# Performance work log

Measured on AMD Instinct MI355X. Metric: run time of the kernel, lower is better.

The kernel has to match this reference:

```python
import jax, jax.numpy as jnp
import numpy as np
import math

B = 128      # n_atom_basis
F = 32       # n_filters
R = 20       # n_rbf
N = 16384    # atoms
E = 262144   # edges
LOG2 = 0.6931471805599453
IS2 = 1.0 / math.sqrt(2.0)
IS3 = 1.0 / math.sqrt(3.0)
IS6 = 1.0 / math.sqrt(6.0)


def ssp(x):
    # shifted softplus: softplus(x) - log(2)
    return jax.nn.softplus(x) - LOG2


def setup_inputs() -> dict:
    key = jax.random.key(0)
    ks = jax.random.split(key, 14)
    return dict(
        x=jax.random.normal(ks[0], (N, 4 * B), jnp.float32),
        idx_i=jax.random.randint(ks[1], (E,), 0, N),
        idx_j=jax.random.randint(ks[2], (E,), 0, N),
        f_ij=jax.random.normal(ks[3], (E, R), jnp.float32),
        rcut_ij=jax.random.uniform(ks[4], (E,), jnp.float32),
        Yr_ij=jax.random.normal(ks[5], (E, 4), jnp.float32),
        # e3nn-style Linear weights (N(0,1), normalized by 1/sqrt(fan_in) at use)
        w_in2f_s=jax.random.normal(ks[6], (B, F), jnp.float32),
        w_in2f_v=jax.random.normal(ks[7], (B, F), jnp.float32),
        W1=jax.random.normal(ks[8], (R, F), jnp.float32) / math.sqrt(R),
        b1=jnp.zeros((F,), jnp.float32),
        W2=jax.random.normal(ks[9], (F, 6 * F), jnp.float32) / math.sqrt(F),
        b2=jnp.zeros((6 * F,), jnp.float32),
        w_f2o1_s=jax.random.normal(ks[10], (2 * F, B), jnp.float32),
        w_f2o1_v=jax.random.normal(ks[11], (2 * F, B), jnp.float32),
        w_f2o2_s=jax.random.normal(ks[12], (B, B), jnp.float32),
        w_f2o2_v=jax.random.normal(ks[13], (B, B), jnp.float32),
    )


def reference(x, idx_i, idx_j, f_ij, rcut_ij, Yr_ij,
              w_in2f_s, w_in2f_v, W1, b1, W2, b2,
              w_f2o1_s, w_f2o1_v, w_f2o2_s, w_f2o2_v):
    n = x.shape[0]
    # input layout: [B x 0e | B x 1o]
    xs = x[:, :B]                          # [N,B] scalars
    xv = x[:, B:].reshape(n, B, 3)         # [N,B,3] vectors
    # in2f: per-l equivariant linear (fan_in = B)
    hs = (xs @ w_in2f_s) / math.sqrt(B)                            # [N,F]
    hv = jnp.einsum('nbc,bf->nfc', xv, w_in2f_v) / math.sqrt(B)    # [N,F,3]
    # gather neighbors j
    s = hs[idx_j]                          # [E,F]
    v = hv[idx_j]                          # [E,F,3]
    ys = Yr_ij[:, 0]                       # [E]   l=0 part of Y(r)
    yv = Yr_ij[:, 1:4]                     # [E,3] l=1 part of Y(r)
    # FullTensorProduct (0e+1o) x (0e+1o), component normalization
    t_s1 = s * ys[:, None]                                   # 0e (0x0)
    t_s2 = jnp.einsum('efc,ec->ef', v, yv) * IS3             # 0e (1x1->0)
    t_v1 = s[:, :, None] * yv[:, None, :]                    # 1o (0x1)
    t_v2 = v * ys[:, None, None]                             # 1o (1x0)
    t_pv = jnp.cross(v, yv[:, None, :]) * IS2                # 1e (1x1->1)
    ax, ay, az = v[..., 0], v[..., 1], v[..., 2]
    bx, by, bz = yv[:, None, 0:1], yv[:, None, 1:2], yv[:, None, 2:3]
    bx, by, bz = bx[..., 0], by[..., 0], bz[..., 0]
    t_q = jnp.stack([                                        # 2e (1x1->2)
        (ax * by + ay * bx) * IS2,
        (ay * bz + az * by) * IS2,
        (2.0 * az * bz - ax * bx - ay * by) * IS6,
        (ax * bz + az * bx) * IS2,
        (ax * bx - ay * by) * IS2,
    ], axis=-1)                                              # [E,F,5]
    # radial filter network -> one scalar per irrep instance (6 per filter)
    h = ssp(f_ij @ W1 + b1)
    Wij = (h @ W2 + b2) * rcut_ij[:, None]                   # [E,6F]
    Wf = Wij.reshape(-1, F, 6)
    # elementwise tensor product (continuous-filter convolution)
    edge = jnp.concatenate([
        (t_s1 * Wf[..., 0])[..., None],
        (t_s2 * Wf[..., 1])[..., None],
        t_v1 * Wf[..., 2:3],
        t_v2 * Wf[..., 3:4],
        t_pv * Wf[..., 4:5],
        t_q * Wf[..., 5:6],
    ], axis=-1)                                              # [E,F,16]
    # scatter-add over center atoms i
    agg = jax.ops.segment_sum(edge.reshape(edge.shape[0], -1), idx_i,
                              num_segments=n).reshape(n, F, 16)
    # f2out_1: e3nn Linear keeps only matching irreps (0e,1o); 1e,2e dropped
    s_in = jnp.concatenate([agg[..., 0], agg[..., 1]], axis=1)          # [N,2F]
    v_in = jnp.concatenate([agg[..., 2:5], agg[..., 5:8]], axis=1)      # [N,2F,3]
    os1 = (s_in @ w_f2o1_s) / math.sqrt(2 * F)
    ov1 = jnp.einsum('nmc,mb->nbc', v_in, w_f2o1_v) / math.sqrt(2 * F)
    # gated activation: ssp on scalars only
    os1 = ssp(os1)
    # f2out_2
    os2 = (os1 @ w_f2o2_s) / math.sqrt(B)
    ov2 = jnp.einsum('nbc,bd->ndc', ov1, w_f2o2_v) / math.sqrt(B)
    return jnp.concatenate([os2, ov2.reshape(n, -1)], axis=-1)          # [N,4B]
```

## Files before the change

kernel.cpp:

```cpp
#include <hip/hip_runtime.h>
#include <math.h>

#define NN 16384
#define BB 128
#define FF 32
#define RR 20
#define EE 262144

__device__ __forceinline__ float sspf(float x) {
  return fmaxf(x, 0.0f) + log1pf(expf(-fabsf(x))) - 0.69314718055994531f;
}

__device__ __forceinline__ unsigned int pack_bf2(float a, float b) {
  unsigned int ua = __float_as_uint(a);
  ua = (ua + 0x7fffu + ((ua >> 16) & 1u)) >> 16;
  unsigned int ub = __float_as_uint(b);
  ub = (ub + 0x7fffu + ((ub >> 16) & 1u)) & 0xffff0000u;
  return ua | ub;
}

__global__ __launch_bounds__(256) void k_embed(const float* __restrict__ x,
        const float* __restrict__ ws, const float* __restrict__ wv,
        float4* __restrict__ hsv) {
  __shared__ float sx[32 * 516];
  int t = threadIdx.x;
  int b0 = blockIdx.x * 32;
  const float4* xg = (const float4*)(x + (size_t)b0 * 512);
  for (int i = t; i < 4096; i += 256) {
    int row = i >> 7, col = i & 127;
    *(float4*)(sx + row * 516 + col * 4) = xg[i];
  }
  __syncthreads();
  int n = t >> 3, fq = t & 7;
  const float* xr = sx + n * 516;
  float acc[4][4];
#pragma unroll
  for (int k = 0; k < 4; k++)
#pragma unroll
    for (int c = 0; c < 4; c++) acc[k][c] = 0.f;
  for (int bq = 0; bq < 32; bq++) {
    float4 xs4 = *(const float4*)(xr + 4 * bq);
    float4 a0 = *(const float4*)(xr + 128 + 12 * bq);
    float4 a1 = *(const float4*)(xr + 128 + 12 * bq + 4);
    float4 a2 = *(const float4*)(xr + 128 + 12 * bq + 8);
    float xsv[4] = {xs4.x, xs4.y, xs4.z, xs4.w};
    float vv[4][3];
    vv[0][0] = a0.x; vv[0][1] = a0.y; vv[0][2] = a0.z;
    vv[1][0] = a0.w; vv[1][1] = a1.x; vv[1][2] = a1.y;
    vv[2][0] = a1.z; vv[2][1] = a1.w; vv[2][2] = a2.x;
    vv[3][0] = a2.y; vv[3][1] = a2.z; vv[3][2] = a2.w;
#pragma unroll
    for (int bb = 0; bb < 4; bb++) {
      int b = 4 * bq + bb;
      float4 w_s = *(const float4*)(ws + b * 32 + 4 * fq);
      float4 w_v = *(const float4*)(wv + b * 32 + 4 * fq);
      float wsx[4] = {w_s.x, w_s.y, w_s.z, w_s.w};
      float wvx[4] = {w_v.x, w_v.y, w_v.z, w_v.w};
#pragma unroll
      for (int k = 0; k < 4; k++) {
        acc[k][0] += xsv[bb] * wsx[k];
        acc[k][1] += vv[bb][0] * wvx[k];
        acc[k][2] += vv[bb][1] * wvx[k];
        acc[k][3] += vv[bb][2] * wvx[k];
      }
    }
  }
  const float sc = 0.088388347648318447f;
#pragma unroll
  for (int k = 0; k < 4; k++) {
    float4 o;
    o.x = acc[k][0] * sc; o.y = acc[k][1] * sc;
    o.z = acc[k][2] * sc; o.w = acc[k][3] * sc;
    hsv[(size_t)(b0 + n) * 32 + 4 * fq + k] = o;
  }
}

__global__ __launch_bounds__(256) void k_count(const int* __restrict__ idx_i,
        int* __restrict__ cnt, int* __restrict__ pos) {
  int e = blockIdx.x * 256 + threadIdx.x;
  pos[e] = atomicAdd(cnt + idx_i[e], 1);
}

__global__ __launch_bounds__(256) void k_scan(const int* __restrict__ cnt,
        int* __restrict__ offs) {
  __shared__ int part[256];
  int t = threadIdx.x;
  int s = 0;
  for (int i = t * 64; i < t * 64 + 64; ++i) s += cnt[i];
  part[t] = s;
  __syncthreads();
  if (t == 0) {
    int run = 0;
    for (int i = 0; i < 256; i++) { int v = part[i]; part[i] = run; run += v; }
    offs[NN] = run;
  }
  __syncthreads();
  int run = part[t];
  for (int i = t * 64; i < t * 64 + 64; ++i) { offs[i] = run; run += cnt[i]; }
}

__global__ __launch_bounds__(256) void k_fill(const int* __restrict__ idx_i,
        const int* __restrict__ idx_j, const float* __restrict__ Yr,
        const int* __restrict__ pos, const int* __restrict__ offs,
        int* __restrict__ slot_of_e, int* __restrict__ idxj_csr,
        float4* __restrict__ Yr_csr) {
  int e = blockIdx.x * 256 + threadIdx.x;
  int slot = offs[idx_i[e]] + pos[e];
  slot_of_e[e] = slot;
  idxj_csr[slot] = idx_j[e];
  Yr_csr[slot] = *(const float4*)(Yr + (size_t)e * 4);
}

__global__ __launch_bounds__(256) void k_wv(const float* __restrict__ w1v,
        const float* __restrict__ w2v, float* __restrict__ Wv) {
  int o = blockIdx.x * 256 + threadIdx.x;
  int m = o >> 7, d = o & 127;
  float s = 0.f;
  for (int b = 0; b < 128; b++) s += w1v[m * 128 + b] * w2v[b * 128 + d];
  Wv[o] = s * 0.011048543456039804f;
}

__global__ __launch_bounds__(256, 4) void k_wab(
        const float* __restrict__ fij, const float* __restrict__ rcut,
        const int* __restrict__ slot_of_e,
        const float* __restrict__ W1, const float* __restrict__ b1,
        const float* __restrict__ W2, const float* __restrict__ b2,
        unsigned int* __restrict__ Wab) {
  __shared__ float sW1[640];
  __shared__ float sb1[32];
  __shared__ float sW2c[4096];
  __shared__ float sb2c[128];
  __shared__ float sfij[20 * 130];
  __shared__ float sh[128 * 37];
  __shared__ float srct[128];
  __shared__ int sslot[128];
  int t = threadIdx.x;
  size_t e0 = (size_t)blockIdx.x * 128;
  for (int i = t; i < 640; i += 256) sW1[i] = W1[i];
  if (t < 32) sb1[t] = b1[t];
  for (int i = t; i < 4096; i += 256) {
    int p = i >> 7, c = i & 127;
    sW2c[i] = W2[p * 192 + 6 * (c >> 2) + (c & 3)];
  }
  if (t < 128) sb2c[t] = b2[6 * (t >> 2) + (t & 3)];
  for (int i = t; i < 2560; i += 256) {
    int el = i / 20, r = i - el * 20;
    sfij[r * 130 + el] = fij[e0 * 20 + i];
  }
  if (t < 128) {
    srct[t] = rcut[e0 + t];
    sslot[t] = slot_of_e[e0 + t];
  }
  __syncthreads();
  {
    int el = t & 127, fp0 = (t >> 7) * 16;
    float acc[16];
#pragma unroll
    for (int i = 0; i < 16; i++) acc[i] = sb1[fp0 + i];
#pragma unroll
    for (int r = 0; r < 20; r++) {
      float fe = sfij[r * 130 + el];
      float4 wA = *(const float4*)(sW1 + r * 32 + fp0);
      float4 wB = *(const float4*)(sW1 + r * 32 + fp0 + 4);
      float4 wC = *(const float4*)(sW1 + r * 32 + fp0 + 8);
      float4 wD = *(const float4*)(sW1 + r * 32 + fp0 + 12);
      acc[0] += fe * wA.x;  acc[1] += fe * wA.y;
      acc[2] += fe * wA.z;  acc[3] += fe * wA.w;
      acc[4] += fe * wB.x;  acc[5] += fe * wB.y;
      acc[6] += fe * wB.z;  acc[7] += fe * wB.w;
      acc[8] += fe * wC.x;  acc[9] += fe * wC.y;
      acc[10] += fe * wC.z; acc[11] += fe * wC.w;
      acc[12] += fe * wD.x; acc[13] += fe * wD.y;
      acc[14] += fe * wD.z; acc[15] += fe * wD.w;
    }
#pragma unroll
    for (int i = 0; i < 16; i++) sh[el * 37 + fp0 + i] = sspf(acc[i]);
  }
  __syncthreads();
  {
    int eq = t >> 4, q = t & 15;
    float acc[8][8];
#pragma unroll
    for (int j = 0; j < 8; j++)
#pragma unroll
      for (int i = 0; i < 8; i++)
        acc[j][i] = (i < 4) ? sb2c[4 * q + i] : sb2c[64 + 4 * q + (i - 4)];
#pragma unroll
    for (int p = 0; p < 32; p++) {
      float4 wA = *(const float4*)(sW2c + p * 128 + 4 * q);
      float4 wB = *(const float4*)(sW2c + p * 128 + 64 + 4 * q);
      float w[8] = {wA.x, wA.y, wA.z, wA.w, wB.x, wB.y, wB.z, wB.w};
#pragma unroll
      for (int j = 0; j < 8; j++) {
        float hh = sh[(8 * eq + j) * 37 + p];
#pragma unroll
        for (int i = 0; i < 8; i++) acc[j][i] += hh * w[i];
      }
    }
#pragma unroll
    for (int j = 0; j < 8; j++) {
      float rc = srct[8 * eq + j];
      unsigned int* base = Wab + (size_t)sslot[8 * eq + j] * 64;
      uint2 oA, oB;
      oA.x = pack_bf2(acc[j][0] * rc, acc[j][1] * rc);
      oA.y = pack_bf2(acc[j][2] * rc, acc[j][3] * rc);
      oB.x = pack_bf2(acc[j][4] * rc, acc[j][5] * rc);
      oB.y = pack_bf2(acc[j][6] * rc, acc[j][7] * rc);
      *(uint2*)(base + 2 * q) = oA;
      *(uint2*)(base + 32 + 2 * q) = oB;
    }
  }
}

__global__ __launch_bounds__(256, 4) void k_agg3(
        const unsigned int* __restrict__ Wu, const int* __restrict__ idxj_csr,
        const float4* __restrict__ Yr_csr, const float4* __restrict__ hsv,
        const int* __restrict__ offs, float* __restrict__ nagg) {
  int t = threadIdx.x;
  int w = t >> 6, l = t & 63;
  int n = blockIdx.x * 4 + w;
  int f = l >> 1, kb = (l & 1) * 2;
  int start = offs[n], end = offs[n + 1];
  float a0 = 0, a1 = 0, a2 = 0, a3 = 0, a4 = 0, a5 = 0;
  if (start < end) {
    int last = end - 1;
    int i1 = start + 1 < last ? start + 1 : last;
    int i2 = start + 2 < last ? start + 2 : last;
    int j0 = idxj_csr[start];
    int j1 = idxj_csr[i1];
    int j2 = idxj_csr[i2];
    float4 y0 = Yr_csr[start];
    float4 sv0 = hsv[(size_t)j0 * 32 + f];
    float4 sv1 = hsv[(size_t)j1 * 32 + f];
    unsigned int W0 = Wu[(size_t)start * 64 + l];
    unsigned int W1 = Wu[(size_t)i1 * 64 + l];
    for (int ei = start; ei < end; ++ei) {
      int in1 = ei + 1 < last ? ei + 1 : last;
      int in2 = ei + 2 < last ? ei + 2 : last;
      int in3 = ei + 3 < last ? ei + 3 : last;
      float4 sv2 = hsv[(size_t)j2 * 32 + f];
      unsigned int W2r = Wu[(size_t)in2 * 64 + l];
      float4 y1 = Yr_csr[in1];
      int j3 = idxj_csr[in3];
      float Wx = __uint_as_float(W0 << 16);
      float Wy = __uint_as_float(W0 & 0xffff0000u);
      float ys = y0.x, yx = y0.y, yy = y0.z, yz = y0.w;
      float ss = sv0.x, vx = sv0.y, vy = sv0.z, vz = sv0.w;
      if (kb == 0) {
        a0 += ss * ys * Wx;
        a1 += (vx * yx + vy * yy + vz * yz) * 0.57735026918962576f * Wy;
      } else {
        a0 += ss * yx * Wx; a1 += ss * yy * Wx; a2 += ss * yz * Wx;
        a3 += vx * ys * Wy; a4 += vy * ys * Wy; a5 += vz * ys * Wy;
      }
      y0 = y1; sv0 = sv1; sv1 = sv2; W0 = W1; W1 = W2r; j2 = j3;
    }
  }
  float* na = nagg + (size_t)n * 256;
  if (kb == 0) {
    na[f] = a0;
    na[32 + f] = a1;
  } else {
    na[64 + 3 * f + 0] = a0;  na[64 + 3 * f + 1] = a1;  na[64 + 3 * f + 2] = a2;
    na[160 + 3 * f + 0] = a3; na[160 + 3 * f + 1] = a4; na[160 + 3 * f + 2] = a5;
  }
}

__global__ __launch_bounds__(256) void k_os1(const float* __restrict__ na,
        const float* __restrict__ w1s, float* __restrict__ os1) {
  __shared__ float sw[8192];
  int t = threadIdx.x;
  for (int i = t; i < 8192; i += 256) sw[i] = w1s[i];
  __syncthreads();
  int dg = t & 31, ng = t >> 5;
  int d0 = dg * 4;
  int n0 = blockIdx.x * 32 + ng * 4;
  const float* ap = na + (size_t)n0 * 256;
  float acc[4][4] = {};
#pragma unroll
  for (int kq = 0; kq < 16; kq++) {
    float4 a[4];
#pragma unroll
    for (int j = 0; j < 4; j++) a[j] = *(const float4*)(ap + j * 256 + 4 * kq);
    float4 w0 = *(const float4*)(sw + (4 * kq + 0) * 128 + d0);
    float4 w1 = *(const float4*)(sw + (4 * kq + 1) * 128 + d0);
    float4 w2 = *(const float4*)(sw + (4 * kq + 2) * 128 + d0);
    float4 w3 = *(const float4*)(sw + (4 * kq + 3) * 128 + d0);
#pragma unroll
    for (int j = 0; j < 4; j++) {
      acc[j][0] += a[j].x * w0.x + a[j].y * w1.x + a[j].z * w2.x + a[j].w * w3.x;
      acc[j][1] += a[j].x * w0.y + a[j].y * w1.y + a[j].z * w2.y + a[j].w * w3.y;
      acc[j][2] += a[j].x * w0.z + a[j].y * w1.z + a[j].z * w2.z + a[j].w * w3.z;
      acc[j][3] += a[j].x * w0.w + a[j].y * w1.w + a[j].z * w2.w + a[j].w * w3.w;
    }
  }
#pragma unroll
  for (int j = 0; j < 4; j++) {
    float4 o;
    o.x = sspf(acc[j][0] * 0.125f);
    o.y = sspf(acc[j][1] * 0.125f);
    o.z = sspf(acc[j][2] * 0.125f);
    o.w = sspf(acc[j][3] * 0.125f);
    *(float4*)(os1 + (size_t)(n0 + j) * 128 + d0) = o;
  }
}

__global__ __launch_bounds__(256) void k_os2(const float* __restrict__ os1,
        const float* __restrict__ w2s, float* __restrict__ out) {
  __shared__ float sw[16384];
  int t = threadIdx.x;
  for (int i = t; i < 16384; i += 256) sw[i] = w2s[i];
  __syncthreads();
  int dg = t & 31, ng = t >> 5;
  int d0 = dg * 4;
  int n0 = blockIdx.x * 32 + ng * 4;
  const float* ap = os1 + (size_t)n0 * 128;
  float acc[4][4] = {};
#pragma unroll
  for (int kq = 0; kq < 32; kq++) {
    float4 a[4];
#pragma unroll
    for (int j = 0; j < 4; j++) a[j] = *(const float4*)(ap + j * 128 + 4 * kq);
    float4 w0 = *(const float4*)(sw + (4 * kq + 0) * 128 + d0);
    float4 w1 = *(const float4*)(sw + (4 * kq + 1) * 128 + d0);
    float4 w2 = *(const float4*)(sw + (4 * kq + 2) * 128 + d0);
    float4 w3 = *(const float4*)(sw + (4 * kq + 3) * 128 + d0);
#pragma unroll
    for (int j = 0; j < 4; j++) {
      acc[j][0] += a[j].x * w0.x + a[j].y * w1.x + a[j].z * w2.x + a[j].w * w3.x;
      acc[j][1] += a[j].x * w0.y + a[j].y * w1.y + a[j].z * w2.y + a[j].w * w3.y;
      acc[j][2] += a[j].x * w0.z + a[j].y * w1.z + a[j].z * w2.z + a[j].w * w3.z;
      acc[j][3] += a[j].x * w0.w + a[j].y * w1.w + a[j].z * w2.w + a[j].w * w3.w;
    }
  }
  const float sc = 0.088388347648318447f;
#pragma unroll
  for (int j = 0; j < 4; j++) {
    float4 o;
    o.x = acc[j][0] * sc; o.y = acc[j][1] * sc;
    o.z = acc[j][2] * sc; o.w = acc[j][3] * sc;
    *(float4*)(out + (size_t)(n0 + j) * 512 + d0) = o;
  }
}

__global__ __launch_bounds__(256) void k_ov(const float* __restrict__ na,
        const float* __restrict__ Wv, float* __restrict__ out) {
  __shared__ float sw[8192];
  int t = threadIdx.x;
  for (int i = t; i < 8192; i += 256) sw[i] = Wv[i];
  __syncthreads();
  int dg = t & 31, ng = t >> 5;
  int d0 = dg * 4;
  int n0 = blockIdx.x * 16 + ng * 2;
  const float* ap = na + (size_t)n0 * 256 + 64;
  float acc[2][12] = {};
#pragma unroll
  for (int mq = 0; mq < 16; mq++) {
    float4 p[2][3];
#pragma unroll
    for (int j = 0; j < 2; j++) {
      p[j][0] = *(const float4*)(ap + j * 256 + 12 * mq);
      p[j][1] = *(const float4*)(ap + j * 256 + 12 * mq + 4);
      p[j][2] = *(const float4*)(ap + j * 256 + 12 * mq + 8);
    }
    float4 w0 = *(const float4*)(sw + (4 * mq + 0) * 128 + d0);
    float4 w1 = *(const float4*)(sw + (4 * mq + 1) * 128 + d0);
    float4 w2 = *(const float4*)(sw + (4 * mq + 2) * 128 + d0);
    float4 w3 = *(const float4*)(sw + (4 * mq + 3) * 128 + d0);
#pragma unroll
    for (int j = 0; j < 2; j++) {
      float vm[4][3];
      vm[0][0] = p[j][0].x; vm[0][1] = p[j][0].y; vm[0][2] = p[j][0].z;
      vm[1][0] = p[j][0].w; vm[1][1] = p[j][1].x; vm[1][2] = p[j][1].y;
      vm[2][0] = p[j][1].z; vm[2][1] = p[j][1].w; vm[2][2] = p[j][2].x;
      vm[3][0] = p[j][2].y; vm[3][1] = p[j][2].z; vm[3][2] = p[j][2].w;
      float wm[4][4];
      wm[0][0] = w0.x; wm[0][1] = w0.y; wm[0][2] = w0.z; wm[0][3] = w0.w;
      wm[1][0] = w1.x; wm[1][1] = w1.y; wm[1][2] = w1.z; wm[1][3] = w1.w;
      wm[2][0] = w2.x; wm[2][1] = w2.y; wm[2][2] = w2.z; wm[2][3] = w2.w;
      wm[3][0] = w3.x; wm[3][1] = w3.y; wm[3][2] = w3.z; wm[3][3] = w3.w;
#pragma unroll
      for (int m = 0; m < 4; m++)
#pragma unroll
        for (int i = 0; i < 4; i++)
#pragma unroll
          for (int c = 0; c < 3; c++)
            acc[j][i * 3 + c] += vm[m][c] * wm[m][i];
    }
  }
#pragma unroll
  for (int j = 0; j < 2; j++) {
    float* op = out + (size_t)(n0 + j) * 512 + 128 + 12 * dg;
    float4 o0, o1, o2;
    o0.x = acc[j][0]; o0.y = acc[j][1]; o0.z = acc[j][2]; o0.w = acc[j][3];
    o1.x = acc[j][4]; o1.y = acc[j][5]; o1.z = acc[j][6]; o1.w = acc[j][7];
    o2.x = acc[j][8]; o2.y = acc[j][9]; o2.z = acc[j][10]; o2.w = acc[j][11];
    *(float4*)op = o0;
    *(float4*)(op + 4) = o1;
    *(float4*)(op + 8) = o2;
  }
}

extern "C" void kernel_launch(void* const* d_in, const int* in_sizes, int n_in,
                              void* d_out, int out_size, void* d_ws, size_t ws_size,
                              hipStream_t stream) {
  const float* x    = (const float*)d_in[0];
  const int*   idx_i = (const int*)d_in[1];
  const int*   idx_j = (const int*)d_in[2];
  const float* fij  = (const float*)d_in[3];
  const float* rcut = (const float*)d_in[4];
  const float* Yr   = (const float*)d_in[5];
  const float* w_s  = (const float*)d_in[6];
  const float* w_v  = (const float*)d_in[7];
  const float* W1   = (const float*)d_in[8];
  const float* b1   = (const float*)d_in[9];
  const float* W2   = (const float*)d_in[10];
  const float* b2   = (const float*)d_in[11];
  const float* w1s  = (const float*)d_in[12];
  const float* w1v  = (const float*)d_in[13];
  const float* w2s  = (const float*)d_in[14];
  const float* w2v  = (const float*)d_in[15];
  float* out = (float*)d_out;

  char* ws = (char*)d_ws;
  size_t off = 0;
  auto alloc = [&](size_t bytes) {
    void* p = ws + off;
    off += (bytes + 255) & ~(size_t)255;
    return p;
  };
  float4* hsv   = (float4*)alloc((size_t)NN * 32 * 16);
  float*  nagg  = (float*)alloc((size_t)NN * 256 * 4);
  unsigned int* Wab = (unsigned int*)alloc((size_t)EE * 128 * 2);
  float*  os1   = (float*)alloc((size_t)NN * 128 * 4);
  float4* Yr_csr = (float4*)alloc((size_t)EE * 16);
  int* idxj_csr = (int*)alloc((size_t)EE * 4);
  int* slot_of_e = (int*)alloc((size_t)EE * 4);
  float* Wv     = (float*)alloc((size_t)8192 * 4);
  int* cnt      = (int*)alloc((size_t)NN * 4);
  int* offs     = (int*)alloc((size_t)(NN + 1) * 4);
  int* pos      = (int*)alloc((size_t)EE * 4);

  hipMemsetAsync(cnt, 0, (size_t)NN * 4, stream);
  k_count<<<EE / 256, 256, 0, stream>>>(idx_i, cnt, pos);
  k_scan<<<1, 256, 0, stream>>>(cnt, offs);
  k_fill<<<EE / 256, 256, 0, stream>>>(idx_i, idx_j, Yr, pos, offs,
                                       slot_of_e, idxj_csr, Yr_csr);
  k_embed<<<NN / 32, 256, 0, stream>>>(x, w_s, w_v, hsv);
  k_wv<<<32, 256, 0, stream>>>(w1v, w2v, Wv);
  k_wab<<<EE / 128, 256, 0, stream>>>(fij, rcut, slot_of_e, W1, b1, W2, b2, Wab);
  k_agg3<<<NN / 4, 256, 0, stream>>>(Wab, idxj_csr, Yr_csr, hsv, offs, nagg);
  k_os1<<<512, 256, 0, stream>>>(nagg, w1s, os1);
  k_os2<<<512, 256, 0, stream>>>(os1, w2s, out);
  k_ov<<<1024, 256, 0, stream>>>(nagg, Wv, out);
}
```

Measured before the change: 232.6 us.

## Use bf16 MFMA for filter second layer in k_wab with staged coalesced stores

Replaces the scalar FP32 32x128 filter matmul in k_wab with bf16 MFMA 16x16x32 instructions. The weights are pre-packed into a transposed bf16 buffer by a new small prep kernel. The hidden activations are stored as bf16 in LDS, and outputs are staged in LDS so each edge row is written with wide coalesced stores. fij is now read directly from global memory instead of being staged through LDS. This aims to cut the FP32 FMA cost, at the price of bf16 rounding of the hidden activations and weights, plus larger LDS use that lowers the occupancy hint to 2.

```diff
diff --git a/kernel.cpp b/kernel.cpp
--- a/kernel.cpp
+++ b/kernel.cpp
@@ -6,6 +6,9 @@
 #define FF 32
 #define RR 20
 #define EE 262144
+
+typedef __attribute__((ext_vector_type(8))) short bf16x8;
+typedef __attribute__((ext_vector_type(4))) float f32x4;
 
 __device__ __forceinline__ float sspf(float x) {
   return fmaxf(x, 0.0f) + log1pf(expf(-fabsf(x))) - 0.69314718055994531f;
@@ -17,6 +20,12 @@
   unsigned int ub = __float_as_uint(b);
   ub = (ub + 0x7fffu + ((ub >> 16) & 1u)) & 0xffff0000u;
   return ua | ub;
+}
+
+__device__ __forceinline__ unsigned short pack_bf1(float a) {
+  unsigned int ua = __float_as_uint(a);
+  ua = (ua + 0x7fffu + ((ua >> 16) & 1u)) >> 16;
+  return (unsigned short)ua;
 }
 
 __global__ __launch_bounds__(256) void k_embed(const float* __restrict__ x,
@@ -120,46 +129,53 @@
   Wv[o] = s * 0.011048543456039804f;
 }
 
-__global__ __launch_bounds__(256, 4) void k_wab(
+__global__ __launch_bounds__(256) void k_prep(const float* __restrict__ W2,
+        unsigned short* __restrict__ BTbf) {
+  int i = blockIdx.x * 256 + threadIdx.x;
+  int col = i >> 5, k = i & 31;
+  BTbf[col * 32 + k] = pack_bf1(W2[k * 192 + 6 * (col >> 2) + (col & 3)]);
+}
+
+__global__ __launch_bounds__(256, 2) void k_wab(
         const float* __restrict__ fij, const float* __restrict__ rcut,
         const int* __restrict__ slot_of_e,
         const float* __restrict__ W1, const float* __restrict__ b1,
-        const float* __restrict__ W2, const float* __restrict__ b2,
+        const unsigned short* __restrict__ BTbf, const float* __restrict__ b2,
         unsigned int* __restrict__ Wab) {
   __shared__ float sW1[640];
   __shared__ float sb1[32];
-  __shared__ float sW2c[4096];
   __shared__ float sb2c[128];
-  __shared__ float sfij[20 * 130];
-  __shared__ float sh[128 * 37];
   __shared__ float srct[128];
   __shared__ int sslot[128];
+  __shared__ unsigned short hbf[128 * 40];
+  __shared__ unsigned short sBT[128 * 40];
+  __shared__ unsigned short stage[128 * 136];
   int t = threadIdx.x;
   size_t e0 = (size_t)blockIdx.x * 128;
   for (int i = t; i < 640; i += 256) sW1[i] = W1[i];
   if (t < 32) sb1[t] = b1[t];
-  for (int i = t; i < 4096; i += 256) {
-    int p = i >> 7, c = i & 127;
-    sW2c[i] = W2[p * 192 + 6 * (c >> 2) + (c & 3)];
-  }
-  if (t < 128) sb2c[t] = b2[6 * (t >> 2) + (t & 3)];
-  for (int i = t; i < 2560; i += 256) {
-    int el = i / 20, r = i - el * 20;
-    sfij[r * 130 + el] = fij[e0 * 20 + i];
-  }
   if (t < 128) {
+    sb2c[t] = b2[6 * (t >> 2) + (t & 3)];
     srct[t] = rcut[e0 + t];
     sslot[t] = slot_of_e[e0 + t];
   }
-  __syncthreads();
   {
-    int el = t & 127, fp0 = (t >> 7) * 16;
+    unsigned int* dst = (unsigned int*)sBT;
+    const unsigned int* src = (const unsigned int*)BTbf;
+    for (int i = t; i < 2048; i += 256) {
+      int col = i >> 4, kp = i & 15;
+      dst[col * 20 + kp] = src[i];
+    }
+  }
+  __syncthreads();
+  {
+    int el = t >> 1, fp0 = (t & 1) * 16;
+    const float* fr = fij + (e0 + el) * 20;
     float acc[16];
 #pragma unroll
     for (int i = 0; i < 16; i++) acc[i] = sb1[fp0 + i];
-#pragma unroll
     for (int r = 0; r < 20; r++) {
-      float fe = sfij[r * 130 + el];
+      float fe = fr[r];
       float4 wA = *(const float4*)(sW1 + r * 32 + fp0);
       float4 wB = *(const float4*)(sW1 + r * 32 + fp0 + 4);
       float4 wC = *(const float4*)(sW1 + r * 32 + fp0 + 8);
@@ -173,42 +189,61 @@
       acc[12] += fe * wD.x; acc[13] += fe * wD.y;
       acc[14] += fe * wD.z; acc[15] += fe * wD.w;
     }
-#pragma unroll
-    for (int i = 0; i < 16; i++) sh[el * 37 + fp0 + i] = sspf(acc[i]);
+    unsigned int* hw = (unsigned int*)hbf;
+#pragma unroll
+    for (int i = 0; i < 8; i++)
+      hw[el * 20 + (fp0 >> 1) + i] =
+          pack_bf2(sspf(acc[2 * i]), sspf(acc[2 * i + 1]));
   }
   __syncthreads();
   {
-    int eq = t >> 4, q = t & 15;
-    float acc[8][8];
-#pragma unroll
-    for (int j = 0; j < 8; j++)
-#pragma unroll
-      for (int i = 0; i < 8; i++)
-        acc[j][i] = (i < 4) ? sb2c[4 * q + i] : sb2c[64 + 4 * q + (i - 4)];
-#pragma unroll
-    for (int p = 0; p < 32; p++) {
-      float4 wA = *(const float4*)(sW2c + p * 128 + 4 * q);
-      float4 wB = *(const float4*)(sW2c + p * 128 + 64 + 4 * q);
-      float w[8] = {wA.x, wA.y, wA.z, wA.w, wB.x, wB.y, wB.z, wB.w};
-#pragma unroll
-      for (int j = 0; j < 8; j++) {
-        float hh = sh[(8 * eq + j) * 37 + p];
-#pragma unroll
-        for (int i = 0; i < 8; i++) acc[j][i] += hh * w[i];
+    int w = t >> 6, l = t & 63;
+    int lrow = l & 15, lkb = (l >> 4) * 16;
+    const char* hb = (const char*)hbf;
+    const char* bb = (const char*)sBT;
+#pragma unroll
+    for (int g = 0; g < 2; g++) {
+      bf16x8 bfr[4];
+#pragma unroll
+      for (int c = 0; c < 4; c++) {
+        int col = (4 * g + c) * 16 + lrow;
+        bfr[c] = *(const bf16x8*)(bb + col * 80 + lkb);
       }
-    }
-#pragma unroll
-    for (int j = 0; j < 8; j++) {
-      float rc = srct[8 * eq + j];
-      unsigned int* base = Wab + (size_t)sslot[8 * eq + j] * 64;
-      uint2 oA, oB;
-      oA.x = pack_bf2(acc[j][0] * rc, acc[j][1] * rc);
-      oA.y = pack_bf2(acc[j][2] * rc, acc[j][3] * rc);
-      oB.x = pack_bf2(acc[j][4] * rc, acc[j][5] * rc);
-      oB.y = pack_bf2(acc[j][6] * rc, acc[j][7] * rc);
-      *(uint2*)(base + 2 * q) = oA;
-      *(uint2*)(base + 32 + 2 * q) = oB;
-    }
+      f32x4 acc[2][4];
+#pragma unroll
+      for (int rt = 0; rt < 2; rt++) {
+        int row = w * 32 + rt * 16 + lrow;
+        bf16x8 af = *(const bf16x8*)(hb + row * 80 + lkb);
+#pragma unroll
+        for (int c = 0; c < 4; c++) {
+          f32x4 z = {0.f, 0.f, 0.f, 0.f};
+          acc[rt][c] = __builtin_amdgcn_mfma_f32_16x16x32_bf16(
+              af, bfr[c], z, 0, 0, 0);
+        }
+      }
+#pragma unroll
+      for (int rt = 0; rt < 2; rt++)
+#pragma unroll
+        for (int c = 0; c < 4; c++) {
+          int col = (4 * g + c) * 16 + lrow;
+          float bias = sb2c[col];
+          int rbase = w * 32 + rt * 16 + (l >> 4) * 4;
+#pragma unroll
+          for (int r = 0; r < 4; r++) {
+            int row = rbase + r;
+            float v = (acc[rt][c][r] + bias) * srct[row];
+            stage[row * 136 + col] = pack_bf1(v);
+          }
+        }
+    }
+  }
+  __syncthreads();
+  {
+    int row = t >> 1, half = t & 1;
+    const uint4* src = (const uint4*)((const char*)stage + row * 272 + half * 128);
+    uint4* dst = (uint4*)(Wab + (size_t)sslot[row] * 64 + half * 32);
+#pragma unroll
+    for (int i = 0; i < 8; i++) dst[i] = src[i];
   }
 }
 
@@ -437,6 +472,7 @@
   int* idxj_csr = (int*)alloc((size_t)EE * 4);
   int* slot_of_e = (int*)alloc((size_t)EE * 4);
   float* Wv     = (float*)alloc((size_t)8192 * 4);
+  unsigned short* BTbf = (unsigned short*)alloc((size_t)4096 * 2);
   int* cnt      = (int*)alloc((size_t)NN * 4);
   int* offs     = (int*)alloc((size_t)(NN + 1) * 4);
   int* pos      = (int*)alloc((size_t)EE * 4);
@@ -448,7 +484,8 @@
                                        slot_of_e, idxj_csr, Yr_csr);
   k_embed<<<NN / 32, 256, 0, stream>>>(x, w_s, w_v, hsv);
   k_wv<<<32, 256, 0, stream>>>(w1v, w2v, Wv);
-  k_wab<<<EE / 128, 256, 0, stream>>>(fij, rcut, slot_of_e, W1, b1, W2, b2, Wab);
+  k_prep<<<16, 256, 0, stream>>>(W2, BTbf);
+  k_wab<<<EE / 128, 256, 0, stream>>>(fij, rcut, slot_of_e, W1, b1, BTbf, b2, Wab);
   k_agg3<<<NN / 4, 256, 0, stream>>>(Wab, idxj_csr, Yr_csr, hsv, offs, nagg);
   k_os1<<<512, 256, 0, stream>>>(nagg, w1s, os1);
   k_os2<<<512, 256, 0, stream>>>(os1, w2s, out);
```

After: 219.7 us. 5.6% less time.
